# Kernel tuning notes

Measured on AMD Instinct MI355X. Metric: run time of the kernel, lower is better.

## Reference

```python
import jax, jax.numpy as jnp
import numpy as np

H, C = 4, 32          # GAT heads, per-head dim
NH = 4                # transformer heads


def layer_norm(x, g, b, eps=1e-5):
    mu = x.mean(-1, keepdims=True)
    var = ((x - mu) ** 2).mean(-1, keepdims=True)
    return (x - mu) / jnp.sqrt(var + eps) * g + b


def setup_inputs() -> dict:
    key = jax.random.key(0)
    ks = jax.random.split(key, 16)
    B, T, N, F = 256, 72, 5, 10
    D, FF = 128, 256
    # full directed graph on 5 stations, no self loops (E=20)
    ei = np.array([[i, j] for i in range(N) for j in range(N) if i != j], dtype=np.int32).T
    s = 0.1
    return {
        'x': jax.random.normal(ks[0], (B, T, N, F), jnp.float32),
        'edge_index': jnp.asarray(ei),
        'gcn_w': jax.random.normal(ks[1], (F, 64), jnp.float32) * s,
        'gcn_b': jnp.zeros((64,), jnp.float32),
        'gat_w': jax.random.normal(ks[2], (64, H * C), jnp.float32) * s,
        'gat_a_src': jax.random.normal(ks[3], (H, C), jnp.float32) * s,
        'gat_a_dst': jax.random.normal(ks[4], (H, C), jnp.float32) * s,
        'gat_b': jnp.zeros((H * C,), jnp.float32),
        'gln_g': jnp.ones((D,), jnp.float32),
        'gln_b': jnp.zeros((D,), jnp.float32),
        'tw_qkv': jax.random.normal(ks[5], (3, D, 3 * D), jnp.float32) * s,
        'tb_qkv': jnp.zeros((3, 3 * D), jnp.float32),
        'tw_o': jax.random.normal(ks[6], (3, D, D), jnp.float32) * s,
        'tb_o': jnp.zeros((3, D), jnp.float32),
        'ln1_g': jnp.ones((3, D), jnp.float32),
        'ln1_b': jnp.zeros((3, D), jnp.float32),
        'w_ff1': jax.random.normal(ks[7], (3, D, FF), jnp.float32) * s,
        'b_ff1': jnp.zeros((3, FF), jnp.float32),
        'w_ff2': jax.random.normal(ks[8], (3, FF, D), jnp.float32) * s,
        'b_ff2': jnp.zeros((3, D), jnp.float32),
        'ln2_g': jnp.ones((3, D), jnp.float32),
        'ln2_b': jnp.zeros((3, D), jnp.float32),
        'hw1': jax.random.normal(ks[9], (6, D, D // 2), jnp.float32) * s,
        'hb1': jnp.zeros((6, D // 2), jnp.float32),
        'hw2': jax.random.normal(ks[10], (6, D // 2, 5), jnp.float32) * s,
        'hb2': jnp.zeros((6, 5), jnp.float32),
    }


def reference(x, edge_index, gcn_w, gcn_b, gat_w, gat_a_src, gat_a_dst, gat_b,
              gln_g, gln_b, tw_qkv, tb_qkv, tw_o, tb_o, ln1_g, ln1_b,
              w_ff1, b_ff1, w_ff2, b_ff2, ln2_g, ln2_b, hw1, hb1, hw2, hb2):
    B, T, N, F = x.shape
    D = gln_g.shape[0]

    # ---- frozen GCN encoder (torch.no_grad): symmetric-normalized A with self loops
    src, dst = edge_index[0], edge_index[1]
    loop = jnp.arange(N, dtype=src.dtype)
    src2 = jnp.concatenate([src, loop])
    dst2 = jnp.concatenate([dst, loop])
    A = jnp.zeros((N, N), x.dtype).at[dst2, src2].add(1.0)
    deg = A.sum(1)
    dinv = jnp.where(deg > 0, deg ** -0.5, 0.0)
    Anorm = dinv[:, None] * A * dinv[None, :]
    xw = jnp.einsum('btnf,fh->btnh', x, gcn_w) + gcn_b
    gcn = jnp.tanh(jnp.einsum('ij,btjh->btih', Anorm, xw))
    gcn = jax.lax.stop_gradient(gcn)  # encoder is frozen + no_grad

    # ---- GATConv over batched graph (self loops added, PyG default), eval mode (no dropout)
    h = jnp.einsum('btnf,fhc->btnhc', gcn, gat_w.reshape(gcn.shape[-1], H, C))
    a_s = (h * gat_a_src).sum(-1)                         # [B,T,N,H]
    a_d = (h * gat_a_dst).sum(-1)
    e = a_s[:, :, src2, :] + a_d[:, :, dst2, :]           # [B,T,E2,H]
    e = jnp.where(e > 0, e, 0.2 * e)                      # LeakyReLU(0.2)
    eT = jnp.moveaxis(e, 2, 0)                            # [E2,B,T,H]
    m = jax.ops.segment_max(eT, dst2, num_segments=N)
    ex = jnp.exp(eT - m[dst2])
    denom = jax.ops.segment_sum(ex, dst2, num_segments=N)
    alpha = ex / denom[dst2]                              # scatter-softmax per dst node
    hsrc = jnp.moveaxis(h, 2, 0)[src2]                    # [E2,B,T,H,C]
    agg = jax.ops.segment_sum(alpha[..., None] * hsrc, dst2, num_segments=N)
    gat = jnp.moveaxis(agg, 0, 2).reshape(B, T, N, H * C) + gat_b
    gat = layer_norm(gat, gln_g, gln_b)

    # ---- mean-pool stations, positional encoding
    z = gat.mean(2)                                       # [B,T,D]
    pos = jnp.arange(T, dtype=jnp.float32)[:, None]
    div = jnp.exp(jnp.arange(0, D, 2, dtype=jnp.float32) * (-np.log(10000.0) / D))
    pe = jnp.zeros((T, D), x.dtype).at[:, 0::2].set(jnp.sin(pos * div)).at[:, 1::2].set(jnp.cos(pos * div))
    z = z + pe

    # ---- post-norm transformer encoder (relu FF), eval mode
    dh = D // NH
    scale = jnp.sqrt(jnp.asarray(dh, x.dtype))
    for i in range(tw_qkv.shape[0]):
        qkv = z @ tw_qkv[i] + tb_qkv[i]
        q, k, v = jnp.split(qkv, 3, axis=-1)
        q = q.reshape(B, T, NH, dh)
        k = k.reshape(B, T, NH, dh)
        v = v.reshape(B, T, NH, dh)
        att = jax.nn.softmax(jnp.einsum('bqhd,bkhd->bhqk', q, k) / scale, axis=-1)
        o = jnp.einsum('bhqk,bkhd->bqhd', att, v).reshape(B, T, D)
        z = layer_norm(z + o @ tw_o[i] + tb_o[i], ln1_g[i], ln1_b[i])
        ff = jax.nn.relu(z @ w_ff1[i] + b_ff1[i]) @ w_ff2[i] + b_ff2[i]
        z = layer_norm(z + ff, ln2_g[i], ln2_b[i])

    # ---- multi-horizon forecast heads on last timestep -> stacked [6,B,5]
    last = z[:, -1]
    h1 = jax.nn.relu(jnp.einsum('bd,kdm->kbm', last, hw1) + hb1[:, None, :])
    out = jnp.einsum('kbm,kms->kbs', h1, hw2) + hb2[:, None, :]
    return out
```

## Files before the change

kernel.cpp:

```cpp
#include <hip/hip_runtime.h>
#include <hip/hip_bf16.h>

#define B_  256
#define T_  72
#define N_  5
#define F_  10
#define D_  128
#define HH_ 4
#define CC_ 32
#define FF_ 256
#define BT_ (B_*T_)
#define E2MAX 32

#define WS_Z    256
#define WS_QKV  (WS_Z + BT_*D_)
#define WS_OBUF (WS_QKV + BT_*3*D_)
#define WS_WBF  (WS_OBUF + BT_*D_)

#define WOFF_QKV(i)  ((i)*49152)
#define WOFF_O(i)    (147456 + (i)*16384)
#define WOFF_FF1(i)  (196608 + (i)*32768)
#define WOFF_FF2(i)  (294912 + (i)*32768)
#define WOFF_GATW    393216

#define MZF_OFF   0
#define MSB_OFF   38016
#define MSQ_OFF   70784
#define MSK_OFF   92544
#define MVT_OFF   114304
#define MOB_OFF   140928
#define MSMEM_BYTES 162688

typedef __attribute__((ext_vector_type(8))) short bf16x8;
typedef __attribute__((ext_vector_type(4))) float f32x4;

__device__ __forceinline__ unsigned short bf16_rne(float x) {
    unsigned u = __float_as_uint(x);
    unsigned r = (u + 0x7FFFu + ((u >> 16) & 1u)) >> 16;
    return (unsigned short)r;
}
__device__ __forceinline__ unsigned bf16pk(float a, float b) {
    return (unsigned)bf16_rne(a) | ((unsigned)bf16_rne(b) << 16);
}
__device__ __forceinline__ float bf2f(short s) {
    return __uint_as_float(((unsigned)(unsigned short)s) << 16);
}
__device__ __forceinline__ bf16x8 cvt8(const float* p) {
    float4 a = *(const float4*)p;
    float4 b = *(const float4*)(p + 4);
    unsigned u[4] = {bf16pk(a.x, a.y), bf16pk(a.z, a.w), bf16pk(b.x, b.y), bf16pk(b.z, b.w)};
    return *(bf16x8*)u;
}

__global__ void setup_kernel(const int* __restrict__ ei, float* __restrict__ ws, int E) {
    if (threadIdx.x != 0 || blockIdx.x != 0) return;
    int* wsi = (int*)ws;
    const int N = N_;
    int E2 = E + N;
    int src2[E2MAX], dst2[E2MAX];
    for (int e = 0; e < E; ++e) { src2[e] = ei[e]; dst2[e] = ei[E + e]; }
    for (int n = 0; n < N; ++n) { src2[E + n] = n; dst2[E + n] = n; }
    float A[N_ * N_];
    for (int i = 0; i < N * N; ++i) A[i] = 0.f;
    for (int e = 0; e < E2; ++e) A[dst2[e] * N + src2[e]] += 1.f;
    float dinv[N_];
    for (int n = 0; n < N; ++n) {
        float s = 0.f;
        for (int j = 0; j < N; ++j) s += A[n * N + j];
        dinv[n] = (s > 0.f) ? rsqrtf(s) : 0.f;
    }
    for (int n = 0; n < N; ++n)
        for (int j = 0; j < N; ++j)
            ws[n * N + j] = dinv[n] * A[n * N + j] * dinv[j];
    int cnt[N_];
    for (int n = 0; n < N; ++n) cnt[n] = 0;
    for (int e = 0; e < E2; ++e) cnt[dst2[e]]++;
    int off = 0;
    for (int n = 0; n < N; ++n) { wsi[96 + n] = off; off += cnt[n]; }
    wsi[96 + N] = off;
    int cur[N_];
    for (int n = 0; n < N; ++n) cur[n] = wsi[96 + n];
    for (int e = 0; e < E2; ++e) wsi[104 + cur[dst2[e]]++] = e;
    for (int e = 0; e < E2; ++e) { wsi[32 + e] = src2[e]; wsi[64 + e] = dst2[e]; }
}

__global__ __launch_bounds__(256) void prep_kernel(
    const float* __restrict__ tw_qkv, const float* __restrict__ tw_o,
    const float* __restrict__ w_ff1, const float* __restrict__ w_ff2,
    const float* __restrict__ gat_w, short* __restrict__ wbf)
{
    __shared__ float s_t[64][65];
    const int tid = threadIdx.x;
    int t = blockIdx.x;
    const float* src; short* dst; int R, C, tr, tc;
    if (t >= 96) { int q = t - 96; src = gat_w; dst = wbf + WOFF_GATW; R = 64; C = 128; tr = 0; tc = q; }
    else {
        int layer = t / 32, r32 = t % 32;
        if (r32 < 12)      { src = tw_qkv + layer * (128*384); dst = wbf + WOFF_QKV(layer); R = 128; C = 384; tr = r32 / 6;  tc = r32 % 6; }
        else if (r32 < 16) { int q = r32 - 12; src = tw_o + layer * 16384; dst = wbf + WOFF_O(layer);  R = 128; C = 128; tr = q >> 1; tc = q & 1; }
        else if (r32 < 24) { int q = r32 - 16; src = w_ff1 + layer * 32768; dst = wbf + WOFF_FF1(layer); R = 128; C = 256; tr = q >> 2; tc = q & 3; }
        else               { int q = r32 - 24; src = w_ff2 + layer * 32768; dst = wbf + WOFF_FF2(layer); R = 256; C = 128; tr = q >> 1; tc = q & 1; }
    }
    #pragma unroll
    for (int it = 0; it < 16; ++it) {
        int e = it * 256 + tid;
        int r = e >> 6, c = e & 63;
        s_t[r][c] = src[(size_t)(tr*64 + r) * C + tc*64 + c];
    }
    __syncthreads();
    #pragma unroll
    for (int it = 0; it < 16; ++it) {
        int e = it * 256 + tid;
        int c = e >> 6, r = e & 63;
        dst[(size_t)(tc*64 + c) * R + tr*64 + r] = (short)bf16_rne(s_t[r][c]);
    }
}

__device__ __forceinline__ bf16x8 ld_frag(const short* s, int row, int kbase, int ldk) {
    return *(const bf16x8*)&s[row * ldk + (kbase ^ ((row & 7) << 3))];
}
__device__ __forceinline__ void stage_b(short* s_b, const short* __restrict__ src, int tid) {
    const uint4* s4 = (const uint4*)src;
    #pragma unroll
    for (int it = 0; it < 8; ++it) {
        int c = it * 256 + tid;
        int row = c >> 4, ke = (c & 15) * 8;
        *(uint4*)&s_b[row * 128 + (ke ^ ((row & 7) << 3))] = s4[c];
    }
}
__device__ __forceinline__ void stage_b512(short* s_b, const short* __restrict__ src, int tid) {
    const uint4* s4 = (const uint4*)src;
    #pragma unroll
    for (int it = 0; it < 4; ++it) {
        int c = it * 512 + tid;
        int row = c >> 4, ke = (c & 15) * 8;
        *(uint4*)&s_b[row * 128 + (ke ^ ((row & 7) << 3))] = s4[c];
    }
}

__global__ __launch_bounds__(256) void gcn_h_mfma(
    const float* __restrict__ x, const float* __restrict__ gcn_w, const float* __restrict__ gcn_b,
    const float* __restrict__ a_src, const float* __restrict__ a_dst,
    const float* __restrict__ ws, const short* __restrict__ gwT,
    short* __restrict__ hbuf, float* __restrict__ asb, float* __restrict__ adb)
{
    __shared__ float s_x[16 * 50];
    __shared__ float s_an[25];
    __shared__ short s_gcn[80 * 64];

    const int tid = threadIdx.x;
    const int tok0 = blockIdx.x * 16;

    for (int i = tid; i < 16 * 50; i += 256) s_x[i] = x[(size_t)tok0 * 50 + i];
    if (tid < 25) s_an[tid] = ws[tid];
    __syncthreads();

    #pragma unroll
    for (int it = 0; it < 2; ++it) {
        int idx = it * 256 + tid;
        int tl = idx >> 5, kp = idx & 31;
        int k0 = kp * 2;
        float w0[F_], w1[F_];
        #pragma unroll
        for (int f = 0; f < F_; ++f) { w0[f] = gcn_w[f * 64 + k0]; w1[f] = gcn_w[f * 64 + k0 + 1]; }
        float b0 = gcn_b[k0], b1 = gcn_b[k0 + 1];
        float xw0[N_], xw1[N_];
        #pragma unroll
        for (int n = 0; n < N_; ++n) {
            float a0 = b0, a1 = b1;
            #pragma unroll
            for (int f = 0; f < F_; ++f) {
                float xv = s_x[tl * 50 + n * 10 + f];
                a0 += xv * w0[f]; a1 += xv * w1[f];
            }
            xw0[n] = a0; xw1[n] = a1;
        }
        #pragma unroll
        for (int n = 0; n < N_; ++n) {
            float s0 = 0.f, s1 = 0.f;
            #pragma unroll
            for (int j = 0; j < N_; ++j) { float an = s_an[n * 5 + j]; s0 += an * xw0[j]; s1 += an * xw1[j]; }
            float e0 = __expf(2.f * fabsf(s0)), e1 = __expf(2.f * fabsf(s1));
            float t0 = copysignf(1.f - 2.f / (e0 + 1.f), s0);
            float t1 = copysignf(1.f - 2.f / (e1 + 1.f), s1);
            int row = tl * 5 + n;
            *(unsigned*)&s_gcn[row * 64 + (k0 ^ ((row & 7) << 3))] = bf16pk(t0, t1);
        }
    }
    __syncthreads();

    const int w = tid >> 6, lane = tid & 63;
    const int c = lane & 15, g = lane >> 4;
    const int kf = g * 8;
    bf16x8 bfr[2][2];
    #pragma unroll
    for (int nn = 0; nn < 2; ++nn)
        #pragma unroll
        for (int k0 = 0; k0 < 2; ++k0)
            bfr[nn][k0] = *(const bf16x8*)&gwT[(w * 32 + nn * 16 + c) * 64 + k0 * 32 + kf];
    const float as0 = a_src[w * 32 + c],      as1 = a_src[w * 32 + 16 + c];
    const float ad0 = a_dst[w * 32 + c],      ad1 = a_dst[w * 32 + 16 + c];
    #pragma unroll
    for (int m = 0; m < 5; ++m) {
        bf16x8 af0 = ld_frag(s_gcn, m * 16 + c, kf, 64);
        bf16x8 af1 = ld_frag(s_gcn, m * 16 + c, 32 + kf, 64);
        f32x4 a0 = {0,0,0,0}, a1 = {0,0,0,0};
        a0 = __builtin_amdgcn_mfma_f32_16x16x32_bf16(af0, bfr[0][0], a0, 0, 0, 0);
        a0 = __builtin_amdgcn_mfma_f32_16x16x32_bf16(af1, bfr[0][1], a0, 0, 0, 0);
        a1 = __builtin_amdgcn_mfma_f32_16x16x32_bf16(af0, bfr[1][0], a1, 0, 0, 0);
        a1 = __builtin_amdgcn_mfma_f32_16x16x32_bf16(af1, bfr[1][1], a1, 0, 0, 0);
        float ps[4], pd[4];
        #pragma unroll
        for (int i = 0; i < 4; ++i) {
            int row = m * 16 + g * 4 + i;
            size_t gr = (size_t)(tok0 * 5 + row) * 128;
            hbuf[gr + w * 32 + c]      = (short)bf16_rne(a0[i]);
            hbuf[gr + w * 32 + 16 + c] = (short)bf16_rne(a1[i]);
            ps[i] = a0[i] * as0 + a1[i] * as1;
            pd[i] = a0[i] * ad0 + a1[i] * ad1;
        }
        #pragma unroll
        for (int mm = 1; mm < 16; mm <<= 1)
            #pragma unroll
            for (int i = 0; i < 4; ++i) { ps[i] += __shfl_xor(ps[i], mm); pd[i] += __shfl_xor(pd[i], mm); }
        if (c == 0) {
            #pragma unroll
            for (int i = 0; i < 4; ++i) {
                int row = m * 16 + g * 4 + i;
                asb[(size_t)(tok0 * 5 + row) * 4 + w] = ps[i];
                adb[(size_t)(tok0 * 5 + row) * 4 + w] = pd[i];
            }
        }
    }
}

__global__ __launch_bounds__(256) void gat_agg(
    const short* __restrict__ hbuf, const float* __restrict__ asb, const float* __restrict__ adb,
    const float* __restrict__ gat_b, const float* __restrict__ gln_g, const float* __restrict__ gln_b,
    const float* __restrict__ ws, float* __restrict__ z, int E2)
{
    __shared__ int   s_src[E2MAX], s_csr_off[N_ + 1], s_csr_e[E2MAX];
    __shared__ float s_alpha[4][E2MAX][4];
    __shared__ short s_h[4 * 5 * 128];

    const int tid = threadIdx.x;
    const int wv = tid >> 6, lane = tid & 63;
    const int tok = blockIdx.x * 4 + wv;
    const int* wsi = (const int*)ws;

    if (tid < E2) { s_src[tid] = wsi[32 + tid]; s_csr_e[tid] = wsi[104 + tid]; }
    if (tid < N_ + 1) s_csr_off[tid] = wsi[96 + tid];
    {
        const uint4* hb4 = (const uint4*)(hbuf + (size_t)blockIdx.x * 4 * 5 * 128);
        uint4* sh4 = (uint4*)s_h;
        #pragma unroll
        for (int it = 0; it < 2; ++it) {
            int i = it * 256 + tid;
            if (i < 320) sh4[i] = hb4[i];
        }
    }
    __syncthreads();

    if (lane < 20) {
        int dn = lane >> 2, head = lane & 3;
        int j0 = s_csr_off[dn], j1 = s_csr_off[dn + 1];
        float adv = adb[(size_t)(tok * 5 + dn) * 4 + head];
        float mx = -1e30f;
        for (int j = j0; j < j1; ++j) {
            int e = s_csr_e[j];
            float ev = asb[(size_t)(tok * 5 + s_src[e]) * 4 + head] + adv;
            ev = ev > 0.f ? ev : 0.2f * ev;
            mx = fmaxf(mx, ev);
        }
        float den = 0.f;
        for (int j = j0; j < j1; ++j) {
            int e = s_csr_e[j];
            float ev = asb[(size_t)(tok * 5 + s_src[e]) * 4 + head] + adv;
            ev = ev > 0.f ? ev : 0.2f * ev;
            float ex = __expf(ev - mx);
            den += ex;
            s_alpha[wv][e][head] = ex;
        }
        float r = 1.f / den;
        for (int j = j0; j < j1; ++j) s_alpha[wv][s_csr_e[j]][head] *= r;
    }
    __syncthreads();

    const int h0 = lane >> 5, h1 = 2 + (lane >> 5);
    const float gb0 = gat_b[lane],      gb1 = gat_b[lane + 64];
    const float gg0 = gln_g[lane],      gg1 = gln_g[lane + 64];
    const float gB0 = gln_b[lane],      gB1 = gln_b[lane + 64];
    float v0[N_], v1[N_];
    #pragma unroll
    for (int n = 0; n < N_; ++n) {
        float a0 = 0.f, a1 = 0.f;
        int j0 = s_csr_off[n], j1 = s_csr_off[n + 1];
        for (int j = j0; j < j1; ++j) {
            int e = s_csr_e[j];
            int rb = (wv * 5 + s_src[e]) * 128;
            a0 += s_alpha[wv][e][h0] * bf2f(s_h[rb + lane]);
            a1 += s_alpha[wv][e][h1] * bf2f(s_h[rb + lane + 64]);
        }
        v0[n] = a0 + gb0; v1[n] = a1 + gb1;
    }
    float r1[N_], r2[N_];
    #pragma unroll
    for (int n = 0; n < N_; ++n) { r1[n] = v0[n] + v1[n]; r2[n] = v0[n]*v0[n] + v1[n]*v1[n]; }
    #pragma unroll
    for (int mm = 1; mm < 64; mm <<= 1)
        #pragma unroll
        for (int n = 0; n < N_; ++n) { r1[n] += __shfl_xor(r1[n], mm); r2[n] += __shfl_xor(r2[n], mm); }
    float z0 = 0.f, z1 = 0.f;
    #pragma unroll
    for (int n = 0; n < N_; ++n) {
        float mu = r1[n] * (1.f / D_);
        float var = r2[n] * (1.f / D_) - mu * mu;
        float rstd = rsqrtf(var + 1e-5f);
        z0 += (v0[n] - mu) * rstd * gg0 + gB0;
        z1 += (v1[n] - mu) * rstd * gg1 + gB1;
    }
    z0 *= (1.f / N_); z1 *= (1.f / N_);
    const float cpe = -9.210340371976184f / (float)D_;
    int t = tok % T_;
    float dv0 = __expf((float)(lane & ~1) * cpe);
    float dv1 = __expf((float)((lane + 64) & ~1) * cpe);
    float ang0 = (float)t * dv0, ang1 = (float)t * dv1;
    z0 += (lane & 1) ? __cosf(ang0) : __sinf(ang0);
    z1 += (lane & 1) ? __cosf(ang1) : __sinf(ang1);
    z[(size_t)tok * D_ + lane] = z0;
    z[(size_t)tok * D_ + 64 + lane] = z1;
}

__global__ __launch_bounds__(512, 1) void layers_fused(
    const float* __restrict__ zg, const short* __restrict__ wbf,
    const float* __restrict__ tb_qkv, const float* __restrict__ tb_o,
    const float* __restrict__ ln1_g, const float* __restrict__ ln1_b,
    const float* __restrict__ b_ff1, const float* __restrict__ b_ff2,
    const float* __restrict__ ln2_g, const float* __restrict__ ln2_b,
    const float* __restrict__ hw1, const float* __restrict__ hb1,
    const float* __restrict__ hw2, const float* __restrict__ hb2,
    float* __restrict__ out)
{
    extern __shared__ char smem[];
    float* s_zf = (float*)(smem + MZF_OFF);
    short* s_b  = (short*)(smem + MSB_OFF);
    short* s_q  = (short*)(smem + MSQ_OFF);
    short* s_k  = (short*)(smem + MSK_OFF);
    short* s_vt = (short*)(smem + MVT_OFF);
    short* s_ob = (short*)(smem + MOB_OFF);
    short* s_f  = s_q;
    short* s_z1 = s_vt;

    const int tid = threadIdx.x;
    const int w = tid >> 6, lane = tid & 63;
    const int c = lane & 15, g = lane >> 4;
    const int kf = g * 8;
    const int b = blockIdx.x;

    for (int idx = tid; idx < 72 * 128; idx += 512) {
        int r = idx >> 7, col = idx & 127;
        s_zf[r * 132 + col] = zg[(size_t)(b * T_ + r) * D_ + col];
    }
    for (int idx = tid; idx < 128 * 32; idx += 512) {
        int ch = idx >> 5, key = 72 + (idx & 31);
        s_vt[ch * 104 + key] = 0;
    }
    __syncthreads();

    for (int L = 0; L < 3; ++L) {
        const short* Wq = wbf + WOFF_QKV(L);
        const short* Wo = wbf + WOFF_O(L);
        const short* W1 = wbf + WOFF_FF1(L);
        const short* W2 = wbf + WOFF_FF2(L);
        const float* bq = tb_qkv + L * 384;
        const float* bo = tb_o + L * D_;
        const float* g1 = ln1_g + L * D_, *be1 = ln1_b + L * D_;
        const float* b1 = b_ff1 + L * FF_, *b2 = b_ff2 + L * D_;
        const float* g2 = ln2_g + L * D_, *be2 = ln2_b + L * D_;

        for (int ch = 0; ch < 3; ++ch) {
            __syncthreads();
            stage_b512(s_b, Wq + ch * 16384, tid);
            __syncthreads();
            const int n0 = w;
            const int brow = n0 * 16 + c;
            bf16x8 Bf[4];
            #pragma unroll
            for (int k0 = 0; k0 < 4; ++k0) Bf[k0] = ld_frag(s_b, brow, k0 * 32 + kf, 128);
            const float bv = bq[ch * 128 + n0 * 16 + c];
            const int wcol = n0 * 16 + c;
            #pragma unroll
            for (int m = 0; m < 5; ++m) {
                int arow = m * 16 + c;
                bool valid = arow < 72;
                bf16x8 Af[4];
                bf16x8 z8 = {0,0,0,0,0,0,0,0};
                #pragma unroll
                for (int k0 = 0; k0 < 4; ++k0)
                    Af[k0] = valid ? cvt8(&s_zf[arow * 132 + k0 * 32 + kf]) : z8;
                f32x4 acc = {bv, bv, bv, bv};
                #pragma unroll
                for (int k0 = 0; k0 < 4; ++k0)
                    acc = __builtin_amdgcn_mfma_f32_16x16x32_bf16(Af[k0], Bf[k0], acc, 0, 0, 0);
                #pragma unroll
                for (int i = 0; i < 4; ++i) {
                    int lrow = m * 16 + g * 4 + i;
                    short v = (short)bf16_rne(acc[i]);
                    if (ch == 0)      s_q[lrow * 136 + wcol] = v;
                    else if (ch == 1) s_k[lrow * 136 + wcol] = v;
                    else              s_vt[wcol * 104 + lrow] = v;
                }
            }
        }
        __syncthreads();

        {
            short* pstrip = s_b + w * (16 * 104);
            for (int t2 = lane; t2 < 16 * 24; t2 += 64) {
                int r = t2 / 24, col = 80 + (t2 % 24);
                pstrip[r * 104 + col] = 0;
            }
            const int h = w & 3;
            const int mlo = (w >> 2) ? 3 : 0;
            const int mhi = (w >> 2) ? 5 : 3;
            const float scale = 0.17677669529663687f;
            for (int m = mlo; m < mhi; ++m) {
                bf16x8 aq = *(const bf16x8*)&s_q[(m * 16 + c) * 136 + h * 32 + kf];
                float ps[5][4], mx[4], den[4];
                #pragma unroll
                for (int i = 0; i < 4; ++i) mx[i] = -1e30f;
                #pragma unroll
                for (int n0 = 0; n0 < 5; ++n0) {
                    bf16x8 bk = *(const bf16x8*)&s_k[(n0 * 16 + c) * 136 + h * 32 + kf];
                    f32x4 z4 = {0,0,0,0};
                    f32x4 accS = __builtin_amdgcn_mfma_f32_16x16x32_bf16(aq, bk, z4, 0, 0, 0);
                    #pragma unroll
                    for (int i = 0; i < 4; ++i) {
                        float s = accS[i] * scale;
                        if (n0 == 4 && c >= 8) s = -1e30f;
                        ps[n0][i] = s;
                        mx[i] = fmaxf(mx[i], s);
                    }
                }
                #pragma unroll
                for (int mm = 1; mm < 16; mm <<= 1)
                    #pragma unroll
                    for (int i = 0; i < 4; ++i) mx[i] = fmaxf(mx[i], __shfl_xor(mx[i], mm));
                #pragma unroll
                for (int i = 0; i < 4; ++i) den[i] = 0.f;
                #pragma unroll
                for (int n0 = 0; n0 < 5; ++n0)
                    #pragma unroll
                    for (int i = 0; i < 4; ++i) { float e = __expf(ps[n0][i] - mx[i]); ps[n0][i] = e; den[i] += e; }
                #pragma unroll
                for (int mm = 1; mm < 16; mm <<= 1)
                    #pragma unroll
                    for (int i = 0; i < 4; ++i) den[i] += __shfl_xor(den[i], mm);
                float rden[4];
                #pragma unroll
                for (int i = 0; i < 4; ++i) rden[i] = 1.f / den[i];
                #pragma unroll
                for (int n0 = 0; n0 < 5; ++n0)
                    #pragma unroll
                    for (int i = 0; i < 4; ++i)
                        pstrip[(g * 4 + i) * 104 + n0 * 16 + c] = (short)bf16_rne(ps[n0][i] * rden[i]);
                f32x4 accO[2] = {{0,0,0,0},{0,0,0,0}};
                #pragma unroll
                for (int kt = 0; kt < 3; ++kt) {
                    bf16x8 ap = *(const bf16x8*)&pstrip[c * 104 + kt * 32 + kf];
                    #pragma unroll
                    for (int n0 = 0; n0 < 2; ++n0) {
                        bf16x8 bv = *(const bf16x8*)&s_vt[(h * 32 + n0 * 16 + c) * 104 + kt * 32 + kf];
                        accO[n0] = __builtin_amdgcn_mfma_f32_16x16x32_bf16(ap, bv, accO[n0], 0, 0, 0);
                    }
                }
                #pragma unroll
                for (int n0 = 0; n0 < 2; ++n0)
                    #pragma unroll
                    for (int i = 0; i < 4; ++i)
                        s_ob[(m * 16 + g * 4 + i) * 136 + h * 32 + n0 * 16 + c] = (short)bf16_rne(accO[n0][i]);
            }
        }
        __syncthreads();

        stage_b512(s_b, Wo, tid);
        __syncthreads();
        if (w < 5) {
            const int m = w;
            bf16x8 Af[4];
            #pragma unroll
            for (int k0 = 0; k0 < 4; ++k0)
                Af[k0] = *(const bf16x8*)&s_ob[(m * 16 + c) * 136 + k0 * 32 + kf];
            f32x4 acc[8];
            #pragma unroll
            for (int n0 = 0; n0 < 8; ++n0) {
                float bv = bo[n0 * 16 + c];
                acc[n0] = (f32x4){bv, bv, bv, bv};
                int brow = n0 * 16 + c;
                #pragma unroll
                for (int k0 = 0; k0 < 4; ++k0) {
                    bf16x8 bfg = ld_frag(s_b, brow, k0 * 32 + kf, 128);
                    acc[n0] = __builtin_amdgcn_mfma_f32_16x16x32_bf16(Af[k0], bfg, acc[n0], 0, 0, 0);
                }
            }
            #pragma unroll
            for (int n0 = 0; n0 < 8; ++n0)
                #pragma unroll
                for (int i = 0; i < 4; ++i) {
                    int row = m * 16 + g * 4 + i;
                    acc[n0][i] += (row < 72) ? s_zf[row * 132 + n0 * 16 + c] : 0.f;
                }
            float s1[4] = {0,0,0,0}, s2[4] = {0,0,0,0};
            #pragma unroll
            for (int n0 = 0; n0 < 8; ++n0)
                #pragma unroll
                for (int i = 0; i < 4; ++i) { float v = acc[n0][i]; s1[i] += v; s2[i] += v * v; }
            #pragma unroll
            for (int mm = 1; mm < 16; mm <<= 1)
                #pragma unroll
                for (int i = 0; i < 4; ++i) { s1[i] += __shfl_xor(s1[i], mm); s2[i] += __shfl_xor(s2[i], mm); }
            #pragma unroll
            for (int i = 0; i < 4; ++i) {
                float mu = s1[i] * (1.f / D_);
                float var = s2[i] * (1.f / D_) - mu * mu;
                float rstd = rsqrtf(var + 1e-5f);
                int row = m * 16 + g * 4 + i;
                #pragma unroll
                for (int n0 = 0; n0 < 8; ++n0) {
                    float v = (acc[n0][i] - mu) * rstd * g1[n0 * 16 + c] + be1[n0 * 16 + c];
                    if (row < 72) s_zf[row * 132 + n0 * 16 + c] = v;
                    s_z1[row * 136 + n0 * 16 + c] = (short)bf16_rne(v);
                }
            }
        }

        for (int ch = 0; ch < 2; ++ch) {
            __syncthreads();
            stage_b512(s_b, W1 + ch * 16384, tid);
            __syncthreads();
            const int n0 = w;
            const int brow = n0 * 16 + c;
            bf16x8 Bf[4];
            #pragma unroll
            for (int k0 = 0; k0 < 4; ++k0) Bf[k0] = ld_frag(s_b, brow, k0 * 32 + kf, 128);
            const float bv = b1[ch * 128 + n0 * 16 + c];
            #pragma unroll
            for (int m = 0; m < 5; ++m) {
                bf16x8 Af[4];
                #pragma unroll
                for (int k0 = 0; k0 < 4; ++k0)
                    Af[k0] = *(const bf16x8*)&s_z1[(m * 16 + c) * 136 + k0 * 32 + kf];
                f32x4 acc = {bv, bv, bv, bv};
                #pragma unroll
                for (int k0 = 0; k0 < 4; ++k0)
                    acc = __builtin_amdgcn_mfma_f32_16x16x32_bf16(Af[k0], Bf[k0], acc, 0, 0, 0);
                #pragma unroll
                for (int i = 0; i < 4; ++i) {
                    int lrow = m * 16 + g * 4 + i;
                    s_f[lrow * 264 + ch * 128 + n0 * 16 + c] = (short)bf16_rne(fmaxf(acc[i], 0.f));
                }
            }
        }

        f32x4 acc2[8];
        #pragma unroll
        for (int n0 = 0; n0 < 8; ++n0) {
            float bv = b2[n0 * 16 + c];
            acc2[n0] = (f32x4){bv, bv, bv, bv};
        }
        for (int kc = 0; kc < 2; ++kc) {
            __syncthreads();
            {
                #pragma unroll
                for (int it = 0; it < 4; ++it) {
                    int cc = it * 512 + tid;
                    int row = cc >> 4, ke = (cc & 15) * 8;
                    uint4 v = *(const uint4*)&W2[row * 256 + kc * 128 + ke];
                    *(uint4*)&s_b[row * 128 + (ke ^ ((row & 7) << 3))] = v;
                }
            }
            __syncthreads();
            if (w < 5) {
                bf16x8 Af[4];
                #pragma unroll
                for (int k0 = 0; k0 < 4; ++k0)
                    Af[k0] = *(const bf16x8*)&s_f[(w * 16 + c) * 264 + kc * 128 + k0 * 32 + kf];
                #pragma unroll
                for (int n0 = 0; n0 < 8; ++n0) {
                    int brow = n0 * 16 + c;
                    #pragma unroll
                    for (int k0 = 0; k0 < 4; ++k0) {
                        bf16x8 bfg = ld_frag(s_b, brow, k0 * 32 + kf, 128);
                        acc2[n0] = __builtin_amdgcn_mfma_f32_16x16x32_bf16(Af[k0], bfg, acc2[n0], 0, 0, 0);
                    }
                }
            }
        }
        if (w < 5) {
            const int m = w;
            #pragma unroll
            for (int n0 = 0; n0 < 8; ++n0)
                #pragma unroll
                for (int i = 0; i < 4; ++i) {
                    int row = m * 16 + g * 4 + i;
                    acc2[n0][i] += (row < 72) ? s_zf[row * 132 + n0 * 16 + c] : 0.f;
                }
            float s1[4] = {0,0,0,0}, s2[4] = {0,0,0,0};
            #pragma unroll
            for (int n0 = 0; n0 < 8; ++n0)
                #pragma unroll
                for (int i = 0; i < 4; ++i) { float v = acc2[n0][i]; s1[i] += v; s2[i] += v * v; }
            #pragma unroll
            for (int mm = 1; mm < 16; mm <<= 1)
                #pragma unroll
                for (int i = 0; i < 4; ++i) { s1[i] += __shfl_xor(s1[i], mm); s2[i] += __shfl_xor(s2[i], mm); }
            #pragma unroll
            for (int i = 0; i < 4; ++i) {
                float mu = s1[i] * (1.f / D_);
                float var = s2[i] * (1.f / D_) - mu * mu;
                float rstd = rsqrtf(var + 1e-5f);
                int row = m * 16 + g * 4 + i;
                if (row < 72)
                    #pragma unroll
                    for (int n0 = 0; n0 < 8; ++n0)
                        s_zf[row * 132 + n0 * 16 + c] =
                            (acc2[n0][i] - mu) * rstd * g2[n0 * 16 + c] + be2[n0 * 16 + c];
            }
        }
    }

    __syncthreads();
    float* s_h1 = (float*)s_b;
    for (int t2 = tid; t2 < 384; t2 += 512) {
        int k = t2 >> 6, j = t2 & 63;
        float acc = hb1[k * 64 + j];
        const float* w1p = hw1 + (size_t)k * D_ * 64 + j;
        for (int d = 0; d < D_; ++d) acc += s_zf[71 * 132 + d] * w1p[d * 64];
        s_h1[k * 64 + j] = fmaxf(acc, 0.f);
    }
    __syncthreads();
    if (tid < 30) {
        int k = tid / 5, s = tid % 5;
        float o = hb2[k * 5 + s];
        const float* w2p = hw2 + (size_t)k * 64 * 5 + s;
        for (int j = 0; j < 64; ++j) o += s_h1[k * 64 + j] * w2p[j * 5];
        out[(size_t)k * (B_ * 5) + b * 5 + s] = o;
    }
}

extern "C" void kernel_launch(void* const* d_in, const int* in_sizes, int n_in,
                              void* d_out, int out_size, void* d_ws, size_t ws_size,
                              hipStream_t stream) {
    const float* x      = (const float*)d_in[0];
    const int*   ei     = (const int*)  d_in[1];
    const float* gcn_w  = (const float*)d_in[2];
    const float* gcn_b  = (const float*)d_in[3];
    const float* gat_w  = (const float*)d_in[4];
    const float* a_src  = (const float*)d_in[5];
    const float* a_dst  = (const float*)d_in[6];
    const float* gat_b  = (const float*)d_in[7];
    const float* gln_g  = (const float*)d_in[8];
    const float* gln_b  = (const float*)d_in[9];
    const float* tw_qkv = (const float*)d_in[10];
    const float* tb_qkv = (const float*)d_in[11];
    const float* tw_o   = (const float*)d_in[12];
    const float* tb_o   = (const float*)d_in[13];
    const float* ln1_g  = (const float*)d_in[14];
    const float* ln1_b  = (const float*)d_in[15];
    const float* w_ff1  = (const float*)d_in[16];
    const float* b_ff1  = (const float*)d_in[17];
    const float* w_ff2  = (const float*)d_in[18];
    const float* b_ff2  = (const float*)d_in[19];
    const float* ln2_g  = (const float*)d_in[20];
    const float* ln2_b  = (const float*)d_in[21];
    const float* hw1    = (const float*)d_in[22];
    const float* hb1    = (const float*)d_in[23];
    const float* hw2    = (const float*)d_in[24];
    const float* hb2    = (const float*)d_in[25];
    float* out = (float*)d_out;
    float* ws  = (float*)d_ws;

    float* z   = ws + WS_Z;
    short* wbf = (short*)(ws + WS_WBF);

    short* hbuf = (short*)(ws + WS_QKV);
    float* asb  = ws + WS_OBUF;
    float* adb  = ws + WS_OBUF + BT_ * 5 * 4;

    const int E = in_sizes[1] / 2;
    const int E2 = E + N_;

    static bool attr_set = false;
    if (!attr_set) {
        hipFuncSetAttribute((const void*)layers_fused,
                            hipFuncAttributeMaxDynamicSharedMemorySize, MSMEM_BYTES);
        attr_set = true;
    }

    setup_kernel<<<1, 64, 0, stream>>>(ei, ws, E);
    prep_kernel<<<98, 256, 0, stream>>>(tw_qkv, tw_o, w_ff1, w_ff2, gat_w, wbf);
    gcn_h_mfma<<<BT_ / 16, 256, 0, stream>>>(x, gcn_w, gcn_b, a_src, a_dst, ws,
                                             wbf + WOFF_GATW, hbuf, asb, adb);
    gat_agg<<<BT_ / 4, 256, 0, stream>>>(hbuf, asb, adb, gat_b, gln_g, gln_b, ws, z, E2);
    layers_fused<<<B_, 512, MSMEM_BYTES, stream>>>(z, wbf, tb_qkv, tb_o,
                                                   ln1_g, ln1_b, b_ff1, b_ff2,
                                                   ln2_g, ln2_b, hw1, hb1, hw2, hb2, out);
}
```

Before: 289.7 us.

## Load GEMM weight fragments directly from global memory and keep bf16 activation copy

The fused transformer kernel stops staging the QKV, output, FF1 and FF2 weight tiles through shared memory. Each wave now loads its B fragments straight from global memory (expected to hit in L2), which removes several staging passes and block barriers per layer. It also keeps a bf16 copy of the activations in shared memory, updated by the layer-norm epilogue, so the QKV GEMM no longer converts fp32 to bf16 on every A-fragment load. The GAT aggregation kernel now stages its per-block attention logits in shared memory instead of re-reading them from global memory inside the softmax loops. The trade-off is more global/L2 traffic for weights, repeated across waves and blocks, in exchange for fewer syncs.

```diff
diff --git a/kernel.cpp b/kernel.cpp
--- a/kernel.cpp
+++ b/kernel.cpp
@@ -44,12 +44,6 @@
 }
 __device__ __forceinline__ float bf2f(short s) {
     return __uint_as_float(((unsigned)(unsigned short)s) << 16);
-}
-__device__ __forceinline__ bf16x8 cvt8(const float* p) {
-    float4 a = *(const float4*)p;
-    float4 b = *(const float4*)(p + 4);
-    unsigned u[4] = {bf16pk(a.x, a.y), bf16pk(a.z, a.w), bf16pk(b.x, b.y), bf16pk(b.z, b.w)};
-    return *(bf16x8*)u;
 }
 
 __global__ void setup_kernel(const int* __restrict__ ei, float* __restrict__ ws, int E) {
@@ -119,24 +113,6 @@
 __device__ __forceinline__ bf16x8 ld_frag(const short* s, int row, int kbase, int ldk) {
     return *(const bf16x8*)&s[row * ldk + (kbase ^ ((row & 7) << 3))];
 }
-__device__ __forceinline__ void stage_b(short* s_b, const short* __restrict__ src, int tid) {
-    const uint4* s4 = (const uint4*)src;
-    #pragma unroll
-    for (int it = 0; it < 8; ++it) {
-        int c = it * 256 + tid;
-        int row = c >> 4, ke = (c & 15) * 8;
-        *(uint4*)&s_b[row * 128 + (ke ^ ((row & 7) << 3))] = s4[c];
-    }
-}
-__device__ __forceinline__ void stage_b512(short* s_b, const short* __restrict__ src, int tid) {
-    const uint4* s4 = (const uint4*)src;
-    #pragma unroll
-    for (int it = 0; it < 4; ++it) {
-        int c = it * 512 + tid;
-        int row = c >> 4, ke = (c & 15) * 8;
-        *(uint4*)&s_b[row * 128 + (ke ^ ((row & 7) << 3))] = s4[c];
-    }
-}
 
 __global__ __launch_bounds__(256) void gcn_h_mfma(
     const float* __restrict__ x, const float* __restrict__ gcn_w, const float* __restrict__ gcn_b,
@@ -242,6 +218,7 @@
     __shared__ int   s_src[E2MAX], s_csr_off[N_ + 1], s_csr_e[E2MAX];
     __shared__ float s_alpha[4][E2MAX][4];
     __shared__ short s_h[4 * 5 * 128];
+    __shared__ float s_asl[4][N_][4], s_adl[4][N_][4];
 
     const int tid = threadIdx.x;
     const int wv = tid >> 6, lane = tid & 63;
@@ -250,6 +227,8 @@
 
     if (tid < E2) { s_src[tid] = wsi[32 + tid]; s_csr_e[tid] = wsi[104 + tid]; }
     if (tid < N_ + 1) s_csr_off[tid] = wsi[96 + tid];
+    if (tid >= 64 && tid < 144) ((float*)s_asl)[tid - 64] = asb[(size_t)blockIdx.x * 80 + tid - 64];
+    if (tid >= 144 && tid < 224) ((float*)s_adl)[tid - 144] = adb[(size_t)blockIdx.x * 80 + tid - 144];
     {
         const uint4* hb4 = (const uint4*)(hbuf + (size_t)blockIdx.x * 4 * 5 * 128);
         uint4* sh4 = (uint4*)s_h;
@@ -264,18 +243,18 @@
     if (lane < 20) {
         int dn = lane >> 2, head = lane & 3;
         int j0 = s_csr_off[dn], j1 = s_csr_off[dn + 1];
-        float adv = adb[(size_t)(tok * 5 + dn) * 4 + head];
+        float adv = s_adl[wv][dn][head];
         float mx = -1e30f;
         for (int j = j0; j < j1; ++j) {
             int e = s_csr_e[j];
-            float ev = asb[(size_t)(tok * 5 + s_src[e]) * 4 + head] + adv;
+            float ev = s_asl[wv][s_src[e]][head] + adv;
             ev = ev > 0.f ? ev : 0.2f * ev;
             mx = fmaxf(mx, ev);
         }
         float den = 0.f;
         for (int j = j0; j < j1; ++j) {
             int e = s_csr_e[j];
-            float ev = asb[(size_t)(tok * 5 + s_src[e]) * 4 + head] + adv;
+            float ev = s_asl[wv][s_src[e]][head] + adv;
             ev = ev > 0.f ? ev : 0.2f * ev;
             float ex = __expf(ev - mx);
             den += ex;
@@ -357,13 +336,20 @@
     const int kf = g * 8;
     const int b = blockIdx.x;
 
-    for (int idx = tid; idx < 72 * 128; idx += 512) {
-        int r = idx >> 7, col = idx & 127;
-        s_zf[r * 132 + col] = zg[(size_t)(b * T_ + r) * D_ + col];
-    }
-    for (int idx = tid; idx < 128 * 32; idx += 512) {
-        int ch = idx >> 5, key = 72 + (idx & 31);
-        s_vt[ch * 104 + key] = 0;
+    for (int idx = tid; idx < 72 * 64; idx += 512) {
+        int r = idx >> 6, c2 = (idx & 63) * 2;
+        float2 v = *(const float2*)&zg[(size_t)(b * T_ + r) * D_ + c2];
+        s_zf[r * 132 + c2]     = v.x;
+        s_zf[r * 132 + c2 + 1] = v.y;
+        *(unsigned*)&s_b[r * 136 + c2] = bf16pk(v.x, v.y);
+    }
+    {
+        int r = 72 + (tid >> 6), cc = (tid & 63) * 2;
+        *(unsigned*)&s_b[r * 136 + cc] = 0;
+    }
+    for (int idx = tid; idx < 128 * 16; idx += 512) {
+        int chn = idx >> 4, key = 72 + (idx & 15) * 2;
+        *(unsigned*)&s_vt[chn * 104 + key] = 0;
     }
     __syncthreads();
 
@@ -378,37 +364,38 @@
         const float* b1 = b_ff1 + L * FF_, *b2 = b_ff2 + L * D_;
         const float* g2 = ln2_g + L * D_, *be2 = ln2_b + L * D_;
 
-        for (int ch = 0; ch < 3; ++ch) {
-            __syncthreads();
-            stage_b512(s_b, Wq + ch * 16384, tid);
-            __syncthreads();
-            const int n0 = w;
-            const int brow = n0 * 16 + c;
-            bf16x8 Bf[4];
-            #pragma unroll
-            for (int k0 = 0; k0 < 4; ++k0) Bf[k0] = ld_frag(s_b, brow, k0 * 32 + kf, 128);
-            const float bv = bq[ch * 128 + n0 * 16 + c];
-            const int wcol = n0 * 16 + c;
+        {
+            const int wcol = w * 16 + c;
+            bf16x8 Bf[3][4];
+            float bv[3];
+            #pragma unroll
+            for (int ch = 0; ch < 3; ++ch) {
+                const short* Wc = Wq + (size_t)(ch * 128 + wcol) * 128;
+                #pragma unroll
+                for (int k0 = 0; k0 < 4; ++k0) Bf[ch][k0] = *(const bf16x8*)&Wc[k0 * 32 + kf];
+                bv[ch] = bq[ch * 128 + wcol];
+            }
             #pragma unroll
             for (int m = 0; m < 5; ++m) {
-                int arow = m * 16 + c;
-                bool valid = arow < 72;
                 bf16x8 Af[4];
-                bf16x8 z8 = {0,0,0,0,0,0,0,0};
                 #pragma unroll
                 for (int k0 = 0; k0 < 4; ++k0)
-                    Af[k0] = valid ? cvt8(&s_zf[arow * 132 + k0 * 32 + kf]) : z8;
-                f32x4 acc = {bv, bv, bv, bv};
-                #pragma unroll
-                for (int k0 = 0; k0 < 4; ++k0)
-                    acc = __builtin_amdgcn_mfma_f32_16x16x32_bf16(Af[k0], Bf[k0], acc, 0, 0, 0);
+                    Af[k0] = *(const bf16x8*)&s_b[(m * 16 + c) * 136 + k0 * 32 + kf];
+                f32x4 aq = {bv[0], bv[0], bv[0], bv[0]};
+                f32x4 ak = {bv[1], bv[1], bv[1], bv[1]};
+                f32x4 av = {bv[2], bv[2], bv[2], bv[2]};
+                #pragma unroll
+                for (int k0 = 0; k0 < 4; ++k0) {
+                    aq = __builtin_amdgcn_mfma_f32_16x16x32_bf16(Af[k0], Bf[0][k0], aq, 0, 0, 0);
+                    ak = __builtin_amdgcn_mfma_f32_16x16x32_bf16(Af[k0], Bf[1][k0], ak, 0, 0, 0);
+                    av = __builtin_amdgcn_mfma_f32_16x16x32_bf16(Af[k0], Bf[2][k0], av, 0, 0, 0);
+                }
                 #pragma unroll
                 for (int i = 0; i < 4; ++i) {
                     int lrow = m * 16 + g * 4 + i;
-                    short v = (short)bf16_rne(acc[i]);
-                    if (ch == 0)      s_q[lrow * 136 + wcol] = v;
-                    else if (ch == 1) s_k[lrow * 136 + wcol] = v;
-                    else              s_vt[wcol * 104 + lrow] = v;
+                    s_q[lrow * 136 + wcol]  = (short)bf16_rne(aq[i]);
+                    s_k[lrow * 136 + wcol]  = (short)bf16_rne(ak[i]);
+                    s_vt[wcol * 104 + lrow] = (short)bf16_rne(av[i]);
                 }
             }
         }
@@ -483,8 +470,6 @@
         }
         __syncthreads();
 
-        stage_b512(s_b, Wo, tid);
-        __syncthreads();
         if (w < 5) {
             const int m = w;
             bf16x8 Af[4];
@@ -494,14 +479,15 @@
             f32x4 acc[8];
             #pragma unroll
             for (int n0 = 0; n0 < 8; ++n0) {
-                float bv = bo[n0 * 16 + c];
-                acc[n0] = (f32x4){bv, bv, bv, bv};
-                int brow = n0 * 16 + c;
+                const short* Wp = Wo + (size_t)(n0 * 16 + c) * 128;
+                float bvv = bo[n0 * 16 + c];
+                f32x4 a = {bvv, bvv, bvv, bvv};
                 #pragma unroll
                 for (int k0 = 0; k0 < 4; ++k0) {
-                    bf16x8 bfg = ld_frag(s_b, brow, k0 * 32 + kf, 128);
-                    acc[n0] = __builtin_amdgcn_mfma_f32_16x16x32_bf16(Af[k0], bfg, acc[n0], 0, 0, 0);
-                }
+                    bf16x8 bfg = *(const bf16x8*)&Wp[k0 * 32 + kf];
+                    a = __builtin_amdgcn_mfma_f32_16x16x32_bf16(Af[k0], bfg, a, 0, 0, 0);
+                }
+                acc[n0] = a;
             }
             #pragma unroll
             for (int n0 = 0; n0 < 8; ++n0)
@@ -533,71 +519,61 @@
                 }
             }
         }
-
-        for (int ch = 0; ch < 2; ++ch) {
-            __syncthreads();
-            stage_b512(s_b, W1 + ch * 16384, tid);
-            __syncthreads();
-            const int n0 = w;
-            const int brow = n0 * 16 + c;
-            bf16x8 Bf[4];
-            #pragma unroll
-            for (int k0 = 0; k0 < 4; ++k0) Bf[k0] = ld_frag(s_b, brow, k0 * 32 + kf, 128);
-            const float bv = b1[ch * 128 + n0 * 16 + c];
-            #pragma unroll
-            for (int m = 0; m < 5; ++m) {
+        __syncthreads();
+
+        {
+            const int wcol = w * 16 + c;
+            #pragma unroll
+            for (int ch = 0; ch < 2; ++ch) {
+                const short* Wp = W1 + (size_t)(ch * 128 + wcol) * 128;
+                bf16x8 Bf[4];
+                #pragma unroll
+                for (int k0 = 0; k0 < 4; ++k0) Bf[k0] = *(const bf16x8*)&Wp[k0 * 32 + kf];
+                const float bvv = b1[ch * 128 + wcol];
+                #pragma unroll
+                for (int m = 0; m < 5; ++m) {
+                    bf16x8 Af[4];
+                    #pragma unroll
+                    for (int k0 = 0; k0 < 4; ++k0)
+                        Af[k0] = *(const bf16x8*)&s_z1[(m * 16 + c) * 136 + k0 * 32 + kf];
+                    f32x4 a = {bvv, bvv, bvv, bvv};
+                    #pragma unroll
+                    for (int k0 = 0; k0 < 4; ++k0)
+                        a = __builtin_amdgcn_mfma_f32_16x16x32_bf16(Af[k0], Bf[k0], a, 0, 0, 0);
+                    #pragma unroll
+                    for (int i = 0; i < 4; ++i) {
+                        int lrow = m * 16 + g * 4 + i;
+                        s_f[lrow * 264 + ch * 128 + wcol] = (short)bf16_rne(fmaxf(a[i], 0.f));
+                    }
+                }
+            }
+        }
+        __syncthreads();
+
+        if (w < 5) {
+            const int m = w;
+            f32x4 acc2[8];
+            #pragma unroll
+            for (int n0 = 0; n0 < 8; ++n0) {
+                float bvv = b2[n0 * 16 + c];
+                acc2[n0] = (f32x4){bvv, bvv, bvv, bvv};
+            }
+            #pragma unroll
+            for (int kc = 0; kc < 2; ++kc) {
                 bf16x8 Af[4];
                 #pragma unroll
                 for (int k0 = 0; k0 < 4; ++k0)
-                    Af[k0] = *(const bf16x8*)&s_z1[(m * 16 + c) * 136 + k0 * 32 + kf];
-                f32x4 acc = {bv, bv, bv, bv};
-                #pragma unroll
-                for (int k0 = 0; k0 < 4; ++k0)
-                    acc = __builtin_amdgcn_mfma_f32_16x16x32_bf16(Af[k0], Bf[k0], acc, 0, 0, 0);
-                #pragma unroll
-                for (int i = 0; i < 4; ++i) {
-                    int lrow = m * 16 + g * 4 + i;
-                    s_f[lrow * 264 + ch * 128 + n0 * 16 + c] = (short)bf16_rne(fmaxf(acc[i], 0.f));
-                }
-            }
-        }
-
-        f32x4 acc2[8];
-        #pragma unroll
-        for (int n0 = 0; n0 < 8; ++n0) {
-            float bv = b2[n0 * 16 + c];
-            acc2[n0] = (f32x4){bv, bv, bv, bv};
-        }
-        for (int kc = 0; kc < 2; ++kc) {
-            __syncthreads();
-            {
-                #pragma unroll
-                for (int it = 0; it < 4; ++it) {
-                    int cc = it * 512 + tid;
-                    int row = cc >> 4, ke = (cc & 15) * 8;
-                    uint4 v = *(const uint4*)&W2[row * 256 + kc * 128 + ke];
-                    *(uint4*)&s_b[row * 128 + (ke ^ ((row & 7) << 3))] = v;
-                }
-            }
-            __syncthreads();
-            if (w < 5) {
-                bf16x8 Af[4];
-                #pragma unroll
-                for (int k0 = 0; k0 < 4; ++k0)
-                    Af[k0] = *(const bf16x8*)&s_f[(w * 16 + c) * 264 + kc * 128 + k0 * 32 + kf];
+                    Af[k0] = *(const bf16x8*)&s_f[(m * 16 + c) * 264 + kc * 128 + k0 * 32 + kf];
                 #pragma unroll
                 for (int n0 = 0; n0 < 8; ++n0) {
-                    int brow = n0 * 16 + c;
+                    const short* Wp = W2 + (size_t)(n0 * 16 + c) * 256 + kc * 128;
                     #pragma unroll
                     for (int k0 = 0; k0 < 4; ++k0) {
-                        bf16x8 bfg = ld_frag(s_b, brow, k0 * 32 + kf, 128);
+                        bf16x8 bfg = *(const bf16x8*)&Wp[k0 * 32 + kf];
                         acc2[n0] = __builtin_amdgcn_mfma_f32_16x16x32_bf16(Af[k0], bfg, acc2[n0], 0, 0, 0);
                     }
                 }
             }
-        }
-        if (w < 5) {
-            const int m = w;
             #pragma unroll
             for (int n0 = 0; n0 < 8; ++n0)
                 #pragma unroll
@@ -620,16 +596,25 @@
                 float var = s2[i] * (1.f / D_) - mu * mu;
                 float rstd = rsqrtf(var + 1e-5f);
                 int row = m * 16 + g * 4 + i;
-                if (row < 72)
-                    #pragma unroll
-                    for (int n0 = 0; n0 < 8; ++n0)
-                        s_zf[row * 132 + n0 * 16 + c] =
-                            (acc2[n0][i] - mu) * rstd * g2[n0 * 16 + c] + be2[n0 * 16 + c];
-            }
-        }
-    }
-
-    __syncthreads();
+                if (row < 72) {
+                    #pragma unroll
+                    for (int n0 = 0; n0 < 8; ++n0) {
+                        float v = (acc2[n0][i] - mu) * rstd * g2[n0 * 16 + c] + be2[n0 * 16 + c];
+                        s_zf[row * 132 + n0 * 16 + c] = v;
+                        s_b[row * 136 + n0 * 16 + c] = (short)bf16_rne(v);
+                    }
+                }
+            }
+        } else {
+            int wl = (w - 5) * 64 + lane;
+            for (int i = wl; i < 512; i += 192) {
+                int r = 72 + (i >> 6), cc = (i & 63) * 2;
+                *(unsigned*)&s_b[r * 136 + cc] = 0;
+            }
+        }
+        __syncthreads();
+    }
+
     float* s_h1 = (float*)s_b;
     for (int t2 = tid; t2 < 384; t2 += 512) {
         int k = t2 >> 6, j = t2 & 63;
```

Result: no change. 287.0 us (-0.9%).
